# Kernel tuning notes

Hardware: AMD Instinct MI355X
Metric: run time of the kernel (lower is better)

## Reference

```python
import jax, jax.numpy as jnp
import numpy as np

EPS = 1e-12  # torch F.normalize eps

def _normalize(x, axis=-1):
    n = jnp.linalg.norm(x, axis=axis, keepdims=True)
    return x / jnp.maximum(n, EPS)

def setup_inputs() -> dict:
    key = jax.random.key(0)
    ks = jax.random.split(key, 6)
    B, D_in, T, Dc, K = 16, 1024, 4096, 8, 1024
    return {
        "z": jax.random.normal(ks[0], (B, D_in, T), jnp.float32),
        "in_w": jax.random.normal(ks[1], (Dc, D_in), jnp.float32) * 0.02,
        "in_b": jax.random.normal(ks[2], (Dc,), jnp.float32) * 0.02,
        "out_w": jax.random.normal(ks[3], (D_in, Dc), jnp.float32) * 0.02,
        "out_b": jax.random.normal(ks[4], (D_in,), jnp.float32) * 0.02,
        "codebook": jax.random.normal(ks[5], (K, Dc), jnp.float32),
    }

def reference(z, in_w, in_b, out_w, out_b, codebook):
    sg = jax.lax.stop_gradient
    # in_proj: kernel-size-1 conv == per-timestep linear. z: [B, D_in, T] -> z_e: [B, Dc, T]
    z_e = jnp.einsum('od,bdt->bot', in_w, z) + in_b[None, :, None]
    zt = jnp.swapaxes(z_e, 1, 2)  # [B, T, Dc]
    B, T, Dc = zt.shape
    # decode_latents: cosine-normalized squared-distance argmin over codebook
    en = _normalize(zt)                      # [B, T, Dc]
    cn = _normalize(codebook)                # [K, Dc]
    dist = (jnp.sum(en * en, -1, keepdims=True)
            - 2.0 * jnp.einsum('btd,kd->btk', en, cn)
            + jnp.sum(cn * cn, -1)[None, None, :])  # [B, T, K]
    indices = jnp.argmax(-dist, axis=-1)     # [B, T] int
    zq_td = codebook[indices]                # [B, T, Dc] (gather from unnormalized codebook)
    # losses (mean over channel+time dims per batch element)
    commitment_loss = jnp.mean((zt - sg(zq_td)) ** 2, axis=(1, 2))
    codebook_loss = jnp.mean((zq_td - sg(zt)) ** 2, axis=(1, 2))
    # rotation trick: R = I - 2 r r^T + 2 q e^T, applied fused (never materialize BxTxDxD)
    e_norm = _normalize(sg(zt))
    q_norm = _normalize(sg(zq_td))
    r = _normalize(e_norm + q_norm)
    scaling = (jnp.linalg.norm(sg(zq_td), axis=-1)
               / jnp.clip(jnp.linalg.norm(sg(zt), axis=-1), 1e-8))[..., None]
    Rz = zt - 2.0 * r * jnp.sum(r * zt, -1, keepdims=True) \
            + 2.0 * q_norm * jnp.sum(e_norm * zt, -1, keepdims=True)
    zq_rot = scaling * Rz                    # [B, T, Dc]
    zq = jnp.swapaxes(zq_rot, 1, 2)          # [B, Dc, T]
    # out_proj
    z_q_out = jnp.einsum('od,bdt->bot', out_w, zq) + out_b[None, :, None]  # [B, D_in, T]
    return (z_q_out, commitment_loss, codebook_loss, indices.astype(jnp.int32), z_e)
```

## Files before the change

### kernel.cpp

```cpp
#include <hip/hip_runtime.h>
#include <math.h>

#define NB   16
#define DIN  1024
#define TT   4096
#define DC   8
#define NK   1024
#define TA   128
#define NTA  (TT/TA)
#define NPG  16
#define KCP  (NK/NPG)
#define OCH  128
#define NOC  (DIN/OCH)
#define T3TILE 512

#define OFF_CL  ((size_t)NB*DIN*TT)
#define OFF_CB  (OFF_CL + NB)
#define OFF_IDX (OFF_CB + NB)
#define OFF_ZE  (OFF_IDX + (size_t)NB*TT)

__global__ __launch_bounds__(512) void vq_kA(const float* __restrict__ z,
    const float* __restrict__ in_w, const float* __restrict__ in_b,
    float* __restrict__ dout)
{
  __shared__ float wt[DIN*DC];
  __shared__ float pacc[4][TA][DC];
  const int tid = threadIdx.x;
  const int tb = blockIdx.x, b = blockIdx.y;
  for (int i = tid; i < DIN*DC; i += 512) {
    const int d = i >> 3, o = i & 7;
    wt[i] = in_w[o*DIN + d];
  }
  __syncthreads();
  const int sub = tid >> 7, tl = tid & 127;
  const int t = tb*TA + tl;
  const int dbase = sub*256;
  const float* zp = z + ((size_t)b*DIN + dbase)*TT + t;
  float acc[DC];
  #pragma unroll
  for (int o = 0; o < DC; ++o) acc[o] = 0.f;
  #pragma unroll 8
  for (int d = 0; d < 256; ++d) {
    const float v = zp[(size_t)d*TT];
    const float4 w0 = *(const float4*)&wt[(dbase+d)*DC];
    const float4 w1 = *(const float4*)&wt[(dbase+d)*DC+4];
    acc[0] = fmaf(v, w0.x, acc[0]);
    acc[1] = fmaf(v, w0.y, acc[1]);
    acc[2] = fmaf(v, w0.z, acc[2]);
    acc[3] = fmaf(v, w0.w, acc[3]);
    acc[4] = fmaf(v, w1.x, acc[4]);
    acc[5] = fmaf(v, w1.y, acc[5]);
    acc[6] = fmaf(v, w1.z, acc[6]);
    acc[7] = fmaf(v, w1.w, acc[7]);
  }
  *(float4*)&pacc[sub][tl][0] = make_float4(acc[0], acc[1], acc[2], acc[3]);
  *(float4*)&pacc[sub][tl][4] = make_float4(acc[4], acc[5], acc[6], acc[7]);
  __syncthreads();
  #pragma unroll
  for (int oo = 0; oo < 2; ++oo) {
    const int o = (tid >> 7) + oo*4;
    float s = pacc[0][tl][o];
    s += pacc[1][tl][o];
    s += pacc[2][tl][o];
    s += pacc[3][tl][o];
    dout[OFF_ZE + ((size_t)b*DC + o)*TT + t] = s + in_b[o];
  }
}

__global__ __launch_bounds__(512) void vq_kB(const float* __restrict__ ze,
    const float* __restrict__ cbk, float* __restrict__ dout,
    float* __restrict__ zq, float* __restrict__ lpart)
{
  __shared__ float cn[NK*DC];
  __shared__ float cn2[NK];
  __shared__ float2 cand[NPG][TA];
  __shared__ float lred[TA];
  const int tid = threadIdx.x;
  const int tb = blockIdx.x, b = blockIdx.y;

  for (int k = tid; k < NK; k += 512) {
    float c[DC];
    const float4 c0 = *(const float4*)&cbk[k*DC];
    const float4 c1 = *(const float4*)&cbk[k*DC+4];
    c[0]=c0.x; c[1]=c0.y; c[2]=c0.z; c[3]=c0.w;
    c[4]=c1.x; c[5]=c1.y; c[6]=c1.z; c[7]=c1.w;
    float ss = 0.f;
    #pragma unroll
    for (int i = 0; i < DC; ++i) ss = fmaf(c[i], c[i], ss);
    const float den = fmaxf(sqrtf(ss), 1e-12f);
    float s2 = 0.f;
    #pragma unroll
    for (int i = 0; i < DC; ++i) { const float v = c[i]/den; cn[k*DC+i] = v; s2 = fmaf(v, v, s2); }
    cn2[k] = s2;
  }
  __syncthreads();

  const int pg = tid >> 5, l = tid & 31;
  const int k0 = pg*KCP;
  float en[4][DC], en2[4];
  #pragma unroll
  for (int m = 0; m < 4; ++m) {
    const int t = tb*TA + l + 32*m;
    float e[DC];
    #pragma unroll
    for (int o = 0; o < DC; ++o) e[o] = ze[((size_t)b*DC + o)*TT + t];
    float se = 0.f;
    #pragma unroll
    for (int i = 0; i < DC; ++i) se = fmaf(e[i], e[i], se);
    const float dene = fmaxf(sqrtf(se), 1e-12f);
    float s2 = 0.f;
    #pragma unroll
    for (int i = 0; i < DC; ++i) { en[m][i] = e[i]/dene; s2 = fmaf(en[m][i], en[m][i], s2); }
    en2[m] = s2;
  }
  float bd[4]; int bk[4];
  #pragma unroll
  for (int m = 0; m < 4; ++m) { bd[m] = 3.4e38f; bk[m] = k0; }
  #pragma unroll 2
  for (int k = 0; k < KCP; ++k) {
    const float4 a0 = *(const float4*)&cn[(k0+k)*DC];
    const float4 a1 = *(const float4*)&cn[(k0+k)*DC+4];
    const float c2 = cn2[k0+k];
    #pragma unroll
    for (int m = 0; m < 4; ++m) {
      float dacc = en[m][0]*a0.x;
      dacc = fmaf(en[m][1], a0.y, dacc);
      dacc = fmaf(en[m][2], a0.z, dacc);
      dacc = fmaf(en[m][3], a0.w, dacc);
      dacc = fmaf(en[m][4], a1.x, dacc);
      dacc = fmaf(en[m][5], a1.y, dacc);
      dacc = fmaf(en[m][6], a1.z, dacc);
      dacc = fmaf(en[m][7], a1.w, dacc);
      const float dist = (en2[m] - 2.0f*dacc) + c2;
      if (dist < bd[m]) { bd[m] = dist; bk[m] = k0 + k; }
    }
  }
  #pragma unroll
  for (int m = 0; m < 4; ++m)
    cand[pg][l + 32*m] = make_float2(bd[m], __float_as_int(bk[m]) ? __int_as_float(bk[m]) : __int_as_float(bk[m]));
  __syncthreads();

  if (tid < TA) {
    const int tl = tid, t = tb*TA + tl;
    float bdm = cand[0][tl].x;
    int bkm = __float_as_int(cand[0][tl].y);
    #pragma unroll
    for (int p = 1; p < NPG; ++p) {
      const float2 c = cand[p][tl];
      if (c.x < bdm) { bdm = c.x; bkm = __float_as_int(c.y); }
    }
    dout[OFF_IDX + (size_t)b*TT + t] = (float)bkm;

    float e[DC], en_[DC];
    #pragma unroll
    for (int o = 0; o < DC; ++o) e[o] = ze[((size_t)b*DC + o)*TT + t];
    float se = 0.f;
    #pragma unroll
    for (int i = 0; i < DC; ++i) se = fmaf(e[i], e[i], se);
    const float ne = sqrtf(se);
    const float dene = fmaxf(ne, 1e-12f);
    #pragma unroll
    for (int i = 0; i < DC; ++i) en_[i] = e[i]/dene;

    float q[DC];
    {
      const float4 q0 = *(const float4*)&cbk[bkm*DC];
      const float4 q1 = *(const float4*)&cbk[bkm*DC+4];
      q[0]=q0.x; q[1]=q0.y; q[2]=q0.z; q[3]=q0.w;
      q[4]=q1.x; q[5]=q1.y; q[6]=q1.z; q[7]=q1.w;
    }
    float cl = 0.f;
    #pragma unroll
    for (int i = 0; i < DC; ++i) { const float d = e[i]-q[i]; cl = fmaf(d, d, cl); }

    float sq = 0.f;
    #pragma unroll
    for (int i = 0; i < DC; ++i) sq = fmaf(q[i], q[i], sq);
    const float nq = sqrtf(sq);
    const float denq = fmaxf(nq, 1e-12f);
    float qn[DC], rr[DC];
    float sr = 0.f;
    #pragma unroll
    for (int i = 0; i < DC; ++i) { qn[i] = q[i]/denq; rr[i] = en_[i]+qn[i]; sr = fmaf(rr[i], rr[i], sr); }
    const float denr = fmaxf(sqrtf(sr), 1e-12f);
    float r_[DC];
    float rdz = 0.f, edz = 0.f;
    #pragma unroll
    for (int i = 0; i < DC; ++i) { r_[i] = rr[i]/denr; rdz = fmaf(r_[i], e[i], rdz); edz = fmaf(en_[i], e[i], edz); }
    const float scal = nq / fmaxf(ne, 1e-8f);
    #pragma unroll
    for (int i = 0; i < DC; ++i) {
      const float v = scal * ((e[i] - 2.0f*r_[i]*rdz) + 2.0f*qn[i]*edz);
      zq[((size_t)b*DC + i)*TT + t] = v;
    }
    lred[tl] = cl;
  }
  __syncthreads();
  for (int s = TA/2; s > 0; s >>= 1) {
    if (tid < s) lred[tid] += lred[tid + s];
    __syncthreads();
  }
  if (tid == 0) lpart[b*NTA + tb] = lred[0];
}

__global__ __launch_bounds__(256) void vq_kC(const float* __restrict__ zq,
    const float* __restrict__ out_w, const float* __restrict__ out_b,
    const float* __restrict__ lpart, float* __restrict__ dout)
{
  __shared__ float wo[OCH*DC];
  __shared__ float ob[OCH];
  const int tid = threadIdx.x;
  const int tb = blockIdx.x, b = blockIdx.y, oc = blockIdx.z;
  const int obase = oc*OCH;
  for (int i = tid; i < OCH*DC; i += 256) wo[i] = out_w[obase*DC + i];
  if (tid < OCH) ob[tid] = out_b[obase + tid];
  __syncthreads();
  const int t = tb*T3TILE + tid*2;
  float zx[DC], zy[DC];
  #pragma unroll
  for (int c = 0; c < DC; ++c) {
    const float2 v = *(const float2*)&zq[((size_t)b*DC + c)*TT + t];
    zx[c] = v.x; zy[c] = v.y;
  }
  float* op = dout + ((size_t)b*DIN + obase)*TT + t;
  #pragma unroll 4
  for (int o = 0; o < OCH; ++o) {
    const float4 w0 = *(const float4*)&wo[o*DC];
    const float4 w1 = *(const float4*)&wo[o*DC+4];
    const float bv = ob[o];
    float s0 = bv, s1 = bv;
    s0 = fmaf(zx[0], w0.x, s0);  s1 = fmaf(zy[0], w0.x, s1);
    s0 = fmaf(zx[1], w0.y, s0);  s1 = fmaf(zy[1], w0.y, s1);
    s0 = fmaf(zx[2], w0.z, s0);  s1 = fmaf(zy[2], w0.z, s1);
    s0 = fmaf(zx[3], w0.w, s0);  s1 = fmaf(zy[3], w0.w, s1);
    s0 = fmaf(zx[4], w1.x, s0);  s1 = fmaf(zy[4], w1.x, s1);
    s0 = fmaf(zx[5], w1.y, s0);  s1 = fmaf(zy[5], w1.y, s1);
    s0 = fmaf(zx[6], w1.z, s0);  s1 = fmaf(zy[6], w1.z, s1);
    s0 = fmaf(zx[7], w1.w, s0);  s1 = fmaf(zy[7], w1.w, s1);
    *(float2*)&op[(size_t)o*TT] = make_float2(s0, s1);
  }
  if (tb == 0 && oc == 0 && tid == 0) {
    float s = 0.f;
    for (int j = 0; j < NTA; ++j) s += lpart[b*NTA + j];
    const float v = s / (float)(TT*DC);
    dout[OFF_CL + b] = v;
    dout[OFF_CB + b] = v;
  }
}

extern "C" void kernel_launch(void* const* d_in, const int* in_sizes, int n_in,
                              void* d_out, int out_size, void* d_ws, size_t ws_size,
                              hipStream_t stream) {
  const float* z     = (const float*)d_in[0];
  const float* in_w  = (const float*)d_in[1];
  const float* in_b  = (const float*)d_in[2];
  const float* out_w = (const float*)d_in[3];
  const float* out_b = (const float*)d_in[4];
  const float* cbk   = (const float*)d_in[5];
  float* out = (float*)d_out;
  float* ws  = (float*)d_ws;
  const float* ze = out + OFF_ZE;

  float* ZQ = ws;
  float* LP = ZQ + (size_t)NB*DC*TT;

  vq_kA<<<dim3(NTA, NB),              512, 0, stream>>>(z, in_w, in_b, out);
  vq_kB<<<dim3(NTA, NB),              512, 0, stream>>>(ze, cbk, out, ZQ, LP);
  vq_kC<<<dim3(TT/T3TILE, NB, NOC),   256, 0, stream>>>(ZQ, out_w, out_b, LP, out);
}
```

Before: 160.9 us.

## Fuse in-proj, VQ argmin, rotation and out-proj into one megakernel

Merges the three kernels into one per-(time tile, batch) block that keeps z_e and the rotated zq in shared memory, reusing one shared buffer for in_w, the normalized codebook and out_w in turn. The global round trips of z_e and zq and two launch boundaries go away, and a tiny kernel finishes the loss reduction. In exchange each block now runs the whole 1024-channel out-projection for its 128 timesteps, and the larger shared memory footprint may limit occupancy and overlap between memory-bound and compute phases.

```diff
diff --git a/kernel.cpp b/kernel.cpp
--- a/kernel.cpp
+++ b/kernel.cpp
@@ -10,73 +10,73 @@
 #define NTA  (TT/TA)
 #define NPG  16
 #define KCP  (NK/NPG)
-#define OCH  128
-#define NOC  (DIN/OCH)
-#define T3TILE 512
 
 #define OFF_CL  ((size_t)NB*DIN*TT)
 #define OFF_CB  (OFF_CL + NB)
 #define OFF_IDX (OFF_CB + NB)
 #define OFF_ZE  (OFF_IDX + (size_t)NB*TT)
 
-__global__ __launch_bounds__(512) void vq_kA(const float* __restrict__ z,
+__global__ __launch_bounds__(512, 4) void vq_mega(const float* __restrict__ z,
     const float* __restrict__ in_w, const float* __restrict__ in_b,
-    float* __restrict__ dout)
+    const float* __restrict__ out_w, const float* __restrict__ out_b,
+    const float* __restrict__ cbk, float* __restrict__ dout,
+    float* __restrict__ lpart)
 {
-  __shared__ float wt[DIN*DC];
-  __shared__ float pacc[4][TA][DC];
+  __shared__ float regA[DIN*DC];
+  __shared__ float regB[4*TA*DC];
+  __shared__ float ze_s[DC*TA];
+  __shared__ float zq_s[DC*TA];
+  __shared__ float cn2[NK];
+  __shared__ float obs[DIN];
+  __shared__ float lred[TA];
+
   const int tid = threadIdx.x;
   const int tb = blockIdx.x, b = blockIdx.y;
+  const int t0 = tb*TA;
+
   for (int i = tid; i < DIN*DC; i += 512) {
     const int d = i >> 3, o = i & 7;
-    wt[i] = in_w[o*DIN + d];
+    regA[i] = in_w[o*DIN + d];
   }
   __syncthreads();
   const int sub = tid >> 7, tl = tid & 127;
-  const int t = tb*TA + tl;
-  const int dbase = sub*256;
-  const float* zp = z + ((size_t)b*DIN + dbase)*TT + t;
-  float acc[DC];
-  #pragma unroll
-  for (int o = 0; o < DC; ++o) acc[o] = 0.f;
-  #pragma unroll 8
-  for (int d = 0; d < 256; ++d) {
-    const float v = zp[(size_t)d*TT];
-    const float4 w0 = *(const float4*)&wt[(dbase+d)*DC];
-    const float4 w1 = *(const float4*)&wt[(dbase+d)*DC+4];
-    acc[0] = fmaf(v, w0.x, acc[0]);
-    acc[1] = fmaf(v, w0.y, acc[1]);
-    acc[2] = fmaf(v, w0.z, acc[2]);
-    acc[3] = fmaf(v, w0.w, acc[3]);
-    acc[4] = fmaf(v, w1.x, acc[4]);
-    acc[5] = fmaf(v, w1.y, acc[5]);
-    acc[6] = fmaf(v, w1.z, acc[6]);
-    acc[7] = fmaf(v, w1.w, acc[7]);
-  }
-  *(float4*)&pacc[sub][tl][0] = make_float4(acc[0], acc[1], acc[2], acc[3]);
-  *(float4*)&pacc[sub][tl][4] = make_float4(acc[4], acc[5], acc[6], acc[7]);
+  {
+    const int dbase = sub*256;
+    const float* zp = z + ((size_t)b*DIN + dbase)*TT + t0 + tl;
+    float acc[DC];
+    #pragma unroll
+    for (int o = 0; o < DC; ++o) acc[o] = 0.f;
+    #pragma unroll 8
+    for (int d = 0; d < 256; ++d) {
+      const float v = zp[(size_t)d*TT];
+      const float4 w0 = *(const float4*)&regA[(dbase+d)*DC];
+      const float4 w1 = *(const float4*)&regA[(dbase+d)*DC+4];
+      acc[0] = fmaf(v, w0.x, acc[0]);
+      acc[1] = fmaf(v, w0.y, acc[1]);
+      acc[2] = fmaf(v, w0.z, acc[2]);
+      acc[3] = fmaf(v, w0.w, acc[3]);
+      acc[4] = fmaf(v, w1.x, acc[4]);
+      acc[5] = fmaf(v, w1.y, acc[5]);
+      acc[6] = fmaf(v, w1.z, acc[6]);
+      acc[7] = fmaf(v, w1.w, acc[7]);
+    }
+    float* pa = &regB[(sub*TA + tl)*DC];
+    *(float4*)&pa[0] = make_float4(acc[0], acc[1], acc[2], acc[3]);
+    *(float4*)&pa[4] = make_float4(acc[4], acc[5], acc[6], acc[7]);
+  }
   __syncthreads();
   #pragma unroll
   for (int oo = 0; oo < 2; ++oo) {
-    const int o = (tid >> 7) + oo*4;
-    float s = pacc[0][tl][o];
-    s += pacc[1][tl][o];
-    s += pacc[2][tl][o];
-    s += pacc[3][tl][o];
-    dout[OFF_ZE + ((size_t)b*DC + o)*TT + t] = s + in_b[o];
-  }
-}
-
-__global__ __launch_bounds__(512) void vq_kB(const float* __restrict__ ze,
-    const float* __restrict__ cbk, float* __restrict__ dout,
-    float* __restrict__ zq, float* __restrict__ lpart)
-{
-  __shared__ float cn[NK*DC];
-  __shared__ float cn2[NK];
-  __shared__ float2 cand[NPG][TA];
-  __shared__ float lred[TA];
-  const int tid = threadIdx.x;
-  const int tb = blockIdx.x, b = blockIdx.y;
+    const int o = sub + oo*4;
+    float s = regB[(0*TA + tl)*DC + o];
+    s += regB[(1*TA + tl)*DC + o];
+    s += regB[(2*TA + tl)*DC + o];
+    s += regB[(3*TA + tl)*DC + o];
+    const float v = s + in_b[o];
+    ze_s[o*TA + tl] = v;
+    dout[OFF_ZE + ((size_t)b*DC + o)*TT + t0 + tl] = v;
+  }
+  __syncthreads();
 
   for (int k = tid; k < NK; k += 512) {
     float c[DC];
@@ -90,70 +90,73 @@
     const float den = fmaxf(sqrtf(ss), 1e-12f);
     float s2 = 0.f;
     #pragma unroll
-    for (int i = 0; i < DC; ++i) { const float v = c[i]/den; cn[k*DC+i] = v; s2 = fmaf(v, v, s2); }
+    for (int i = 0; i < DC; ++i) { const float v = c[i]/den; regA[k*DC+i] = v; s2 = fmaf(v, v, s2); }
     cn2[k] = s2;
   }
   __syncthreads();
 
-  const int pg = tid >> 5, l = tid & 31;
-  const int k0 = pg*KCP;
-  float en[4][DC], en2[4];
-  #pragma unroll
-  for (int m = 0; m < 4; ++m) {
-    const int t = tb*TA + l + 32*m;
-    float e[DC];
-    #pragma unroll
-    for (int o = 0; o < DC; ++o) e[o] = ze[((size_t)b*DC + o)*TT + t];
-    float se = 0.f;
-    #pragma unroll
-    for (int i = 0; i < DC; ++i) se = fmaf(e[i], e[i], se);
-    const float dene = fmaxf(sqrtf(se), 1e-12f);
-    float s2 = 0.f;
-    #pragma unroll
-    for (int i = 0; i < DC; ++i) { en[m][i] = e[i]/dene; s2 = fmaf(en[m][i], en[m][i], s2); }
-    en2[m] = s2;
-  }
-  float bd[4]; int bk[4];
-  #pragma unroll
-  for (int m = 0; m < 4; ++m) { bd[m] = 3.4e38f; bk[m] = k0; }
-  #pragma unroll 2
-  for (int k = 0; k < KCP; ++k) {
-    const float4 a0 = *(const float4*)&cn[(k0+k)*DC];
-    const float4 a1 = *(const float4*)&cn[(k0+k)*DC+4];
-    const float c2 = cn2[k0+k];
+  {
+    const int pg = tid >> 5, l = tid & 31;
+    const int k0 = pg*KCP;
+    float en[4][DC], en2v[4];
     #pragma unroll
     for (int m = 0; m < 4; ++m) {
-      float dacc = en[m][0]*a0.x;
-      dacc = fmaf(en[m][1], a0.y, dacc);
-      dacc = fmaf(en[m][2], a0.z, dacc);
-      dacc = fmaf(en[m][3], a0.w, dacc);
-      dacc = fmaf(en[m][4], a1.x, dacc);
-      dacc = fmaf(en[m][5], a1.y, dacc);
-      dacc = fmaf(en[m][6], a1.z, dacc);
-      dacc = fmaf(en[m][7], a1.w, dacc);
-      const float dist = (en2[m] - 2.0f*dacc) + c2;
-      if (dist < bd[m]) { bd[m] = dist; bk[m] = k0 + k; }
-    }
-  }
-  #pragma unroll
-  for (int m = 0; m < 4; ++m)
-    cand[pg][l + 32*m] = make_float2(bd[m], __float_as_int(bk[m]) ? __int_as_float(bk[m]) : __int_as_float(bk[m]));
+      const int t = l + 32*m;
+      float e[DC];
+      #pragma unroll
+      for (int o = 0; o < DC; ++o) e[o] = ze_s[o*TA + t];
+      float se = 0.f;
+      #pragma unroll
+      for (int i = 0; i < DC; ++i) se = fmaf(e[i], e[i], se);
+      const float dene = fmaxf(sqrtf(se), 1e-12f);
+      float s2 = 0.f;
+      #pragma unroll
+      for (int i = 0; i < DC; ++i) { en[m][i] = e[i]/dene; s2 = fmaf(en[m][i], en[m][i], s2); }
+      en2v[m] = s2;
+    }
+    float bd[4]; int bk[4];
+    #pragma unroll
+    for (int m = 0; m < 4; ++m) { bd[m] = 3.4e38f; bk[m] = k0; }
+    #pragma unroll 2
+    for (int k = 0; k < KCP; ++k) {
+      const float4 a0 = *(const float4*)&regA[(k0+k)*DC];
+      const float4 a1 = *(const float4*)&regA[(k0+k)*DC+4];
+      const float c2 = cn2[k0+k];
+      #pragma unroll
+      for (int m = 0; m < 4; ++m) {
+        float dacc = en[m][0]*a0.x;
+        dacc = fmaf(en[m][1], a0.y, dacc);
+        dacc = fmaf(en[m][2], a0.z, dacc);
+        dacc = fmaf(en[m][3], a0.w, dacc);
+        dacc = fmaf(en[m][4], a1.x, dacc);
+        dacc = fmaf(en[m][5], a1.y, dacc);
+        dacc = fmaf(en[m][6], a1.z, dacc);
+        dacc = fmaf(en[m][7], a1.w, dacc);
+        const float dist = (en2v[m] - 2.0f*dacc) + c2;
+        if (dist < bd[m]) { bd[m] = dist; bk[m] = k0 + k; }
+      }
+    }
+    float2* cand = (float2*)regB;
+    #pragma unroll
+    for (int m = 0; m < 4; ++m)
+      cand[pg*TA + l + 32*m] = make_float2(bd[m], __int_as_float(bk[m]));
+  }
   __syncthreads();
 
   if (tid < TA) {
-    const int tl = tid, t = tb*TA + tl;
-    float bdm = cand[0][tl].x;
-    int bkm = __float_as_int(cand[0][tl].y);
+    const float2* cand = (const float2*)regB;
+    float bdm = cand[tid].x;
+    int bkm = __float_as_int(cand[tid].y);
     #pragma unroll
     for (int p = 1; p < NPG; ++p) {
-      const float2 c = cand[p][tl];
+      const float2 c = cand[p*TA + tid];
       if (c.x < bdm) { bdm = c.x; bkm = __float_as_int(c.y); }
     }
-    dout[OFF_IDX + (size_t)b*TT + t] = (float)bkm;
+    dout[OFF_IDX + (size_t)b*TT + t0 + tid] = (float)bkm;
 
     float e[DC], en_[DC];
     #pragma unroll
-    for (int o = 0; o < DC; ++o) e[o] = ze[((size_t)b*DC + o)*TT + t];
+    for (int o = 0; o < DC; ++o) e[o] = ze_s[o*TA + tid];
     float se = 0.f;
     #pragma unroll
     for (int i = 0; i < DC; ++i) se = fmaf(e[i], e[i], se);
@@ -191,9 +194,13 @@
     #pragma unroll
     for (int i = 0; i < DC; ++i) {
       const float v = scal * ((e[i] - 2.0f*r_[i]*rdz) + 2.0f*qn[i]*edz);
-      zq[((size_t)b*DC + i)*TT + t] = v;
-    }
-    lred[tl] = cl;
+      zq_s[i*TA + tid] = v;
+    }
+    lred[tid] = cl;
+  } else {
+    const int ti = tid - TA;
+    for (int i = ti; i < DIN*DC; i += 512-TA) regA[i] = out_w[i];
+    for (int i = ti; i < DIN; i += 512-TA) obs[i] = out_b[i];
   }
   __syncthreads();
   for (int s = TA/2; s > 0; s >>= 1) {
@@ -201,45 +208,41 @@
     __syncthreads();
   }
   if (tid == 0) lpart[b*NTA + tb] = lred[0];
+
+  {
+    const int sub3 = tid >> 6, tl2 = tid & 63;
+    const int obase = sub3*128;
+    const int tt2 = tl2*2;
+    float zx[DC], zy[DC];
+    #pragma unroll
+    for (int c = 0; c < DC; ++c) {
+      zx[c] = zq_s[c*TA + tt2];
+      zy[c] = zq_s[c*TA + tt2 + 1];
+    }
+    float* op = dout + ((size_t)b*DIN + obase)*TT + t0 + tt2;
+    #pragma unroll 4
+    for (int o = 0; o < 128; ++o) {
+      const float4 w0 = *(const float4*)&regA[(obase+o)*DC];
+      const float4 w1 = *(const float4*)&regA[(obase+o)*DC+4];
+      const float bv = obs[obase+o];
+      float s0 = bv, s1 = bv;
+      s0 = fmaf(zx[0], w0.x, s0);  s1 = fmaf(zy[0], w0.x, s1);
+      s0 = fmaf(zx[1], w0.y, s0);  s1 = fmaf(zy[1], w0.y, s1);
+      s0 = fmaf(zx[2], w0.z, s0);  s1 = fmaf(zy[2], w0.z, s1);
+      s0 = fmaf(zx[3], w0.w, s0);  s1 = fmaf(zy[3], w0.w, s1);
+      s0 = fmaf(zx[4], w1.x, s0);  s1 = fmaf(zy[4], w1.x, s1);
+      s0 = fmaf(zx[5], w1.y, s0);  s1 = fmaf(zy[5], w1.y, s1);
+      s0 = fmaf(zx[6], w1.z, s0);  s1 = fmaf(zy[6], w1.z, s1);
+      s0 = fmaf(zx[7], w1.w, s0);  s1 = fmaf(zy[7], w1.w, s1);
+      *(float2*)&op[(size_t)o*TT] = make_float2(s0, s1);
+    }
+  }
 }
 
-__global__ __launch_bounds__(256) void vq_kC(const float* __restrict__ zq,
-    const float* __restrict__ out_w, const float* __restrict__ out_b,
-    const float* __restrict__ lpart, float* __restrict__ dout)
+__global__ void vq_fin(const float* __restrict__ lpart, float* __restrict__ dout)
 {
-  __shared__ float wo[OCH*DC];
-  __shared__ float ob[OCH];
-  const int tid = threadIdx.x;
-  const int tb = blockIdx.x, b = blockIdx.y, oc = blockIdx.z;
-  const int obase = oc*OCH;
-  for (int i = tid; i < OCH*DC; i += 256) wo[i] = out_w[obase*DC + i];
-  if (tid < OCH) ob[tid] = out_b[obase + tid];
-  __syncthreads();
-  const int t = tb*T3TILE + tid*2;
-  float zx[DC], zy[DC];
-  #pragma unroll
-  for (int c = 0; c < DC; ++c) {
-    const float2 v = *(const float2*)&zq[((size_t)b*DC + c)*TT + t];
-    zx[c] = v.x; zy[c] = v.y;
-  }
-  float* op = dout + ((size_t)b*DIN + obase)*TT + t;
-  #pragma unroll 4
-  for (int o = 0; o < OCH; ++o) {
-    const float4 w0 = *(const float4*)&wo[o*DC];
-    const float4 w1 = *(const float4*)&wo[o*DC+4];
-    const float bv = ob[o];
-    float s0 = bv, s1 = bv;
-    s0 = fmaf(zx[0], w0.x, s0);  s1 = fmaf(zy[0], w0.x, s1);
-    s0 = fmaf(zx[1], w0.y, s0);  s1 = fmaf(zy[1], w0.y, s1);
-    s0 = fmaf(zx[2], w0.z, s0);  s1 = fmaf(zy[2], w0.z, s1);
-    s0 = fmaf(zx[3], w0.w, s0);  s1 = fmaf(zy[3], w0.w, s1);
-    s0 = fmaf(zx[4], w1.x, s0);  s1 = fmaf(zy[4], w1.x, s1);
-    s0 = fmaf(zx[5], w1.y, s0);  s1 = fmaf(zy[5], w1.y, s1);
-    s0 = fmaf(zx[6], w1.z, s0);  s1 = fmaf(zy[6], w1.z, s1);
-    s0 = fmaf(zx[7], w1.w, s0);  s1 = fmaf(zy[7], w1.w, s1);
-    *(float2*)&op[(size_t)o*TT] = make_float2(s0, s1);
-  }
-  if (tb == 0 && oc == 0 && tid == 0) {
+  const int b = threadIdx.x;
+  if (b < NB) {
     float s = 0.f;
     for (int j = 0; j < NTA; ++j) s += lpart[b*NTA + j];
     const float v = s / (float)(TT*DC);
@@ -258,13 +261,8 @@
   const float* out_b = (const float*)d_in[4];
   const float* cbk   = (const float*)d_in[5];
   float* out = (float*)d_out;
-  float* ws  = (float*)d_ws;
-  const float* ze = out + OFF_ZE;
-
-  float* ZQ = ws;
-  float* LP = ZQ + (size_t)NB*DC*TT;
-
-  vq_kA<<<dim3(NTA, NB),              512, 0, stream>>>(z, in_w, in_b, out);
-  vq_kB<<<dim3(NTA, NB),              512, 0, stream>>>(ze, cbk, out, ZQ, LP);
-  vq_kC<<<dim3(TT/T3TILE, NB, NOC),   256, 0, stream>>>(ZQ, out_w, out_b, LP, out);
+  float* LP  = (float*)d_ws;
+
+  vq_mega<<<dim3(NTA, NB), 512, 0, stream>>>(z, in_w, in_b, out_w, out_b, cbk, out, LP);
+  vq_fin <<<1, 256, 0, stream>>>(LP, out);
 }
```

Measured after the change: 140.1 us. 12.9% less time.
